# Performance work log

Hardware: AMD Instinct MI355X
Metric: run time of the kernel (lower is better)

Reference implementation:

```python
import jax, jax.numpy as jnp
import numpy as np

N_NODES = 200000
N_EDGES = 6400000
N_GRAPHS = 512
VOCAB = 10
EMBED = 8
RLEN = 20
EPS = 1e-5


def setup_inputs() -> dict:
    key = jax.random.key(0)
    ks = jax.random.split(key, 16)
    f = lambda i, shape, s: jax.random.normal(ks[i], shape, jnp.float32) * s
    return {
        "x": jax.random.normal(ks[0], (N_NODES, 3), jnp.float32),
        "W1": f(1, (3, 64), 0.5), "b1": jnp.zeros((64,), jnp.float32),
        "gamma1": jnp.ones((64,), jnp.float32), "beta1": jnp.zeros((64,), jnp.float32),
        "W2": f(2, (64, 64), 0.12), "b2": jnp.zeros((64,), jnp.float32),
        "gamma2": jnp.ones((64,), jnp.float32), "beta2": jnp.zeros((64,), jnp.float32),
        "emb": f(3, (VOCAB, EMBED), 1.0),
        "conv_w": f(4, (16, EMBED, 3), 0.2), "conv_b": jnp.zeros((16,), jnp.float32),
        "fc_w": f(5, (16 * RLEN, 64), 0.06), "fc_b": jnp.zeros((64,), jnp.float32),
        "m1_w": f(6, (192, 128), 0.08), "m1_b": jnp.zeros((128,), jnp.float32),
        "m2_w": f(7, (128, 64), 0.1), "m2_b": jnp.zeros((64,), jnp.float32),
        "m3_w": f(8, (64, 3), 0.17), "m3_b": jnp.zeros((3,), jnp.float32),
        "edge_index": jax.random.randint(ks[9], (2, N_EDGES), 0, N_NODES),
        "batch": jnp.sort(jax.random.randint(ks[10], (N_NODES,), 0, N_GRAPHS)),
        "recipe": jax.random.randint(ks[11], (N_GRAPHS, RLEN), 0, VOCAB),
    }


def _gcn_aggregate(h, src, dst, dinv, n):
    # symmetric-normalized scatter-add: sum_j (d_i d_j)^{-1/2} h_j
    norm = dinv[src] * dinv[dst]
    return jax.ops.segment_sum(h[src] * norm[:, None], dst, num_segments=n)


def _bn(h, gamma, beta):
    mu = h.mean(0)
    var = h.var(0)  # biased variance, as torch BN uses for normalization
    return (h - mu) * jax.lax.rsqrt(var + EPS) * gamma + beta


def reference(x, W1, b1, gamma1, beta1, W2, b2, gamma2, beta2, emb,
              conv_w, conv_b, fc_w, fc_b, m1_w, m1_b, m2_w, m2_b, m3_w, m3_b,
              edge_index, batch, recipe):
    n = x.shape[0]
    loop = jnp.arange(n)
    src = jnp.concatenate([edge_index[0], loop])  # add self loops (GCNConv default)
    dst = jnp.concatenate([edge_index[1], loop])
    deg = jax.ops.segment_sum(jnp.ones_like(src, jnp.float32), dst, num_segments=n)
    dinv = jnp.where(deg > 0, jax.lax.rsqrt(deg), 0.0)

    h = _gcn_aggregate(x @ W1, src, dst, dinv, n) + b1
    h = jax.nn.relu(_bn(h, gamma1, beta1))
    h = _gcn_aggregate(h @ W2, src, dst, dinv, n) + b2
    h = jax.nn.relu(_bn(h, gamma2, beta2))

    counts = jax.ops.segment_sum(jnp.ones((n,), jnp.float32), batch, num_segments=N_GRAPHS)
    h_mean = jax.ops.segment_sum(h, batch, num_segments=N_GRAPHS) / jnp.maximum(counts, 1.0)[:, None]
    h_max = jax.ops.segment_max(h, batch, num_segments=N_GRAPHS)
    h_max = jnp.where(jnp.isfinite(h_max), h_max, 0.0)  # guard empty graphs
    h_graph = jnp.concatenate([h_mean, h_max], axis=1)  # [G, 128]

    r = emb[recipe].transpose(0, 2, 1)  # [G, embed, L]
    rc = jax.lax.conv_general_dilated(r, conv_w, window_strides=(1,), padding=[(1, 1)],
                                      dimension_numbers=("NCH", "OIH", "NCH"))
    rc = jax.nn.relu(rc + conv_b[None, :, None])  # [G, 16, L]
    r_flat = rc.reshape(rc.shape[0], -1)  # channel-major flatten, matches torch
    r_vec = jax.nn.relu(r_flat @ fc_w + fc_b)  # [G, 64]

    c = jnp.concatenate([h_graph, r_vec], axis=1)  # [G, 192]
    c = jax.nn.relu(c @ m1_w + m1_b)
    c = jax.nn.relu(c @ m2_w + m2_b)
    return c @ m3_w + m3_b  # [G, 3]
```

## Files before the change

### kernel.cpp

```cpp
#include <hip/hip_runtime.h>

#define N_NODES 200000
#define N_EDGES 6400000
#define N_GRAPHS 512
#define RLEN 20
#define EMBED 8
#define EPS 1e-5f

#define NPB 1024
#define NBKT ((N_NODES + NPB - 1) / NPB)
#define CHUNK 4096

typedef unsigned short ushort_t;
typedef __attribute__((ext_vector_type(8))) short short8;
typedef __attribute__((ext_vector_type(4))) float f32x4;

__device__ inline ushort_t f32_to_bf16(float f) {
  unsigned u = __float_as_uint(f);
  unsigned r = (u + 0x7fff + ((u >> 16) & 1)) >> 16;
  return (ushort_t)r;
}
__device__ inline float bf16_to_f32(ushort_t us) {
  return __uint_as_float(((unsigned)us) << 16);
}
__device__ inline float bfu_lo(unsigned u) { return __uint_as_float(u << 16); }
__device__ inline float bfu_hi(unsigned u) { return __uint_as_float(u & 0xFFFF0000u); }


__global__ void k_bcount(const int* __restrict__ dst, int* __restrict__ bcnt) {
  __shared__ int hist[NBKT];
  for (int i = threadIdx.x; i < NBKT; i += blockDim.x) hist[i] = 0;
  __syncthreads();
  for (int e = blockIdx.x * blockDim.x + threadIdx.x; e < N_EDGES; e += gridDim.x * blockDim.x)
    atomicAdd(&hist[dst[e] >> 10], 1);
  __syncthreads();
  for (int i = threadIdx.x; i < NBKT; i += blockDim.x)
    if (hist[i]) atomicAdd(&bcnt[i], hist[i]);
}

__global__ void k_bscan(const int* __restrict__ bcnt, int* __restrict__ bstart,
                        int* __restrict__ bcursor, int* __restrict__ rowstart) {
  __shared__ int sb[256];
  int t = threadIdx.x;
  int v = (t < NBKT) ? bcnt[t] : 0;
  sb[t] = v;
  __syncthreads();
  for (int off = 1; off < 256; off <<= 1) {
    int u = (t >= off) ? sb[t - off] : 0;
    __syncthreads();
    sb[t] += u;
    __syncthreads();
  }
  if (t < NBKT) {
    int excl = sb[t] - v;
    bstart[t] = excl;
    bcursor[t] = excl;
  }
  if (t == 0) { bstart[NBKT] = N_EDGES; rowstart[N_NODES] = N_EDGES; }
}

__global__ void __launch_bounds__(256) k_bscatter(const int* __restrict__ src,
                                                  const int* __restrict__ dst,
                                                  int* __restrict__ bcursor,
                                                  int* __restrict__ ebuf) {
  __shared__ int hist[256];
  __shared__ int scanb[256];
  __shared__ int gbase[NBKT];
  __shared__ int staged[CHUNK];
  __shared__ int addrs[CHUNK];
  __shared__ int s_total;
  int t = threadIdx.x;
  int e0 = blockIdx.x * CHUNK;
  hist[t] = 0;
  __syncthreads();

  int pk[16], bk[16], rk[16];
  #pragma unroll
  for (int k = 0; k < 16; ++k) {
    int idx = e0 + t + k * 256;
    bk[k] = -1;
    if (idx < N_EDGES) {
      int s = src[idx], d = dst[idx];
      int b = d >> 10;
      pk[k] = s | ((d & (NPB - 1)) << 18);
      bk[k] = b;
      rk[k] = atomicAdd(&hist[b], 1);
    }
  }
  __syncthreads();
  int hv = hist[t];
  scanb[t] = hv;
  __syncthreads();
  for (int off = 1; off < 256; off <<= 1) {
    int u = (t >= off) ? scanb[t - off] : 0;
    __syncthreads();
    scanb[t] += u;
    __syncthreads();
  }
  int offt = scanb[t] - hv;
  if (t < NBKT && hv > 0) gbase[t] = atomicAdd(&bcursor[t], hv);
  if (t == 255) s_total = scanb[255];
  __syncthreads();
  hist[t] = offt;
  __syncthreads();
  #pragma unroll
  for (int k = 0; k < 16; ++k) {
    if (bk[k] >= 0) {
      int slot = hist[bk[k]] + rk[k];
      staged[slot] = pk[k];
      addrs[slot] = gbase[bk[k]] + rk[k];
    }
  }
  __syncthreads();
  int total = s_total;
  for (int i = t; i < total; i += 256)
    ebuf[addrs[i]] = staged[i];
}

__global__ void __launch_bounds__(256) k_bfill(const int* __restrict__ bstart,
                                               const int* __restrict__ ebuf,
                                               const float* __restrict__ x,
                                               int* __restrict__ rowstart,
                                               float* __restrict__ dinv,
                                               float4* __restrict__ xs,
                                               int* __restrict__ cols) {
  __shared__ int deg[NPB];
  __shared__ int cur[NPB];
  __shared__ int wsum[4];
  int b = blockIdx.x;
  int t = threadIdx.x;
  int lane = t & 63, wid = t >> 6;
  int estart = bstart[b], eend = bstart[b + 1];
  for (int i = t; i < NPB; i += 256) deg[i] = 0;
  __syncthreads();
  for (int i = estart + t; i < eend; i += 256) {
    int p = ebuf[i];
    atomicAdd(&deg[((unsigned)p) >> 18], 1);
  }
  __syncthreads();
  int d0 = deg[t * 4], d1 = deg[t * 4 + 1], d2 = deg[t * 4 + 2], d3 = deg[t * 4 + 3];
  int tsum = d0 + d1 + d2 + d3;
  int incl = tsum;
  #pragma unroll
  for (int off = 1; off < 64; off <<= 1) {
    int u = __shfl_up(incl, off);
    if (lane >= off) incl += u;
  }
  if (lane == 63) wsum[wid] = incl;
  int wexcl = incl - tsum;
  __syncthreads();
  int wbase = 0;
  for (int w = 0; w < wid; ++w) wbase += wsum[w];
  int ebase = wbase + wexcl;
  cur[t * 4 + 0] = ebase;
  cur[t * 4 + 1] = ebase + d0;
  cur[t * 4 + 2] = ebase + d0 + d1;
  cur[t * 4 + 3] = ebase + d0 + d1 + d2;
  __syncthreads();
  #pragma unroll
  for (int k = 0; k < 4; ++k) {
    int dl = t * 4 + k;
    int n = b * NPB + dl;
    if (n < N_NODES) {
      rowstart[n] = estart + cur[dl];
      float dv = rsqrtf((float)(deg[dl] + 1));
      dinv[n] = dv;
      float4 v;
      v.x = x[n * 3 + 0] * dv;
      v.y = x[n * 3 + 1] * dv;
      v.z = x[n * 3 + 2] * dv;
      v.w = 0.f;
      xs[n] = v;
    }
  }
  __syncthreads();
  for (int i = estart + t; i < eend; i += 256) {
    int p = ebuf[i];
    int dl = ((unsigned)p) >> 18;
    int lpos = atomicAdd(&cur[dl], 1);
    cols[estart + lpos] = p & 0x3FFFF;
  }
}


__global__ void k_agg1(const float4* __restrict__ xs, float4* __restrict__ t,
                       const int* __restrict__ rowstart, const int* __restrict__ cols,
                       const float* __restrict__ dinv) {
  int n = blockIdx.x * blockDim.x + threadIdx.x;
  if (n >= N_NODES) return;
  float4 self = xs[n];
  float a0 = self.x, a1 = self.y, a2 = self.z;
  float b0 = 0.f, b1 = 0.f, b2 = 0.f;
  float c0 = 0.f, c1 = 0.f, c2 = 0.f;
  float e0 = 0.f, e1 = 0.f, e2 = 0.f;
  int base = rowstart[n];
  int len = rowstart[n + 1] - base;
  int j = 0;
  for (; j + 4 <= len; j += 4) {
    int s0 = cols[base + j], s1 = cols[base + j + 1];
    int s2 = cols[base + j + 2], s3 = cols[base + j + 3];
    float4 v0 = xs[s0], v1 = xs[s1], v2 = xs[s2], v3 = xs[s3];
    a0 += v0.x; a1 += v0.y; a2 += v0.z;
    b0 += v1.x; b1 += v1.y; b2 += v1.z;
    c0 += v2.x; c1 += v2.y; c2 += v2.z;
    e0 += v3.x; e1 += v3.y; e2 += v3.z;
  }
  for (; j < len; ++j) {
    float4 v = xs[cols[base + j]];
    a0 += v.x; a1 += v.y; a2 += v.z;
  }
  float dv = dinv[n];
  float4 o;
  o.x = dv * ((a0 + b0) + (c0 + e0));
  o.y = dv * ((a1 + b1) + (c1 + e1));
  o.z = dv * ((a2 + b2) + (c2 + e2));
  o.w = 0.f;
  t[n] = o;
}

__global__ void k_mom(const float4* __restrict__ t, float* __restrict__ mom) {
  float m[9] = {0.f, 0.f, 0.f, 0.f, 0.f, 0.f, 0.f, 0.f, 0.f};
  for (int n = blockIdx.x * blockDim.x + threadIdx.x; n < N_NODES; n += gridDim.x * blockDim.x) {
    float4 v = t[n];
    m[0] += v.x; m[1] += v.y; m[2] += v.z;
    m[3] += v.x * v.x; m[4] += v.x * v.y; m[5] += v.x * v.z;
    m[6] += v.y * v.y; m[7] += v.y * v.z; m[8] += v.z * v.z;
  }
  #pragma unroll
  for (int off = 32; off; off >>= 1) {
    #pragma unroll
    for (int i = 0; i < 9; ++i) m[i] += __shfl_xor(m[i], off);
  }
  __shared__ float ls[4][9];
  int lane = threadIdx.x & 63, wid = threadIdx.x >> 6;
  if (lane == 0) {
    #pragma unroll
    for (int i = 0; i < 9; ++i) ls[wid][i] = m[i];
  }
  __syncthreads();
  if (threadIdx.x < 9) {
    float s = ls[0][threadIdx.x] + ls[1][threadIdx.x] + ls[2][threadIdx.x] + ls[3][threadIdx.x];
    atomicAdd(&mom[threadIdx.x], s);
  }
}

__global__ void __launch_bounds__(256) k_l2m2(const float4* __restrict__ t,
                                              ushort_t* __restrict__ hb,
                                              const float* __restrict__ W1,
                                              const float* __restrict__ W2,
                                              const float* __restrict__ mom,
                                              const float* __restrict__ gamma,
                                              const float* __restrict__ beta,
                                              const float* __restrict__ dinv) {
  __shared__ float w1s[192];
  __shared__ ushort_t w2t_hi[64 * 64];
  __shared__ ushort_t w2t_lo[64 * 64];
  __shared__ float tt[4][16][4];
  __shared__ ushort_t at_hi[4][16 * 64];
  __shared__ ushort_t at_lo[4][16 * 64];
  int tix = threadIdx.x;
  int lane = tix & 63, wid = tix >> 6;
  if (tix < 192) w1s[tix] = W1[tix];
  for (int i = tix; i < 64 * 64; i += 256) {
    int f = i >> 6, k = i & 63;
    float w = W2[k * 64 + f];
    ushort_t hi = f32_to_bf16(w);
    w2t_hi[i] = hi;
    w2t_lo[i] = f32_to_bf16(w - bf16_to_f32(hi));
  }
  __syncthreads();

  int col = lane & 15, kb = lane >> 4;
  short8 bhi[4][2], blo[4][2];
  #pragma unroll
  for (int nt = 0; nt < 4; ++nt) {
    #pragma unroll
    for (int ks = 0; ks < 2; ++ks) {
      int base = (nt * 16 + col) * 64 + ks * 32 + kb * 8;
      bhi[nt][ks] = *reinterpret_cast<const short8*>(&w2t_hi[base]);
      blo[nt][ks] = *reinterpret_cast<const short8*>(&w2t_lo[base]);
    }
  }

  float inv_n = 1.0f / N_NODES;
  float w0 = w1s[lane], w1 = w1s[64 + lane], w2 = w1s[128 + lane];
  float mu = (mom[0] * w0 + mom[1] * w1 + mom[2] * w2) * inv_n;
  float eh2 = (mom[3] * w0 * w0 + 2.f * mom[4] * w0 * w1 + 2.f * mom[5] * w0 * w2 +
               mom[6] * w1 * w1 + 2.f * mom[7] * w1 * w2 + mom[8] * w2 * w2) * inv_n;
  float var = eh2 - mu * mu;
  float sc = rsqrtf(var + EPS) * gamma[lane];
  float sh = beta[lane] - mu * sc;

  for (int bt = blockIdx.x; bt < 3125; bt += gridDim.x) {
    int n0 = (bt * 4 + wid) * 16;
    if (lane < 16) {
      float4 v = t[n0 + lane];
      tt[wid][lane][0] = v.x; tt[wid][lane][1] = v.y; tt[wid][lane][2] = v.z;
    }
    #pragma unroll 4
    for (int i = 0; i < 16; ++i) {
      float h = tt[wid][i][0] * w0 + tt[wid][i][1] * w1 + tt[wid][i][2] * w2;
      float a = h * sc + sh;
      a = a > 0.f ? a : 0.f;
      ushort_t hi = f32_to_bf16(a);
      at_hi[wid][i * 64 + lane] = hi;
      at_lo[wid][i * 64 + lane] = f32_to_bf16(a - bf16_to_f32(hi));
    }
    short8 ahi[2], alo[2];
    #pragma unroll
    for (int ks = 0; ks < 2; ++ks) {
      int base = col * 64 + ks * 32 + kb * 8;
      ahi[ks] = *reinterpret_cast<const short8*>(&at_hi[wid][base]);
      alo[ks] = *reinterpret_cast<const short8*>(&at_lo[wid][base]);
    }
    float dv[4];
    #pragma unroll
    for (int r = 0; r < 4; ++r) dv[r] = dinv[n0 + kb * 4 + r];

    #pragma unroll
    for (int nt = 0; nt < 4; ++nt) {
      f32x4 acc = {0.f, 0.f, 0.f, 0.f};
      #pragma unroll
      for (int ks = 0; ks < 2; ++ks) {
        acc = __builtin_amdgcn_mfma_f32_16x16x32_bf16(ahi[ks], bhi[nt][ks], acc, 0, 0, 0);
        acc = __builtin_amdgcn_mfma_f32_16x16x32_bf16(ahi[ks], blo[nt][ks], acc, 0, 0, 0);
        acc = __builtin_amdgcn_mfma_f32_16x16x32_bf16(alo[ks], bhi[nt][ks], acc, 0, 0, 0);
      }
      #pragma unroll
      for (int r = 0; r < 4; ++r) {
        int node = n0 + kb * 4 + r;
        int feat = nt * 16 + col;
        hb[node * 64 + feat] = f32_to_bf16(acc[r] * dv[r]);
      }
    }
  }
}

__global__ void k_agg2(const ushort_t* __restrict__ hb, float* __restrict__ hout,
                       const int* __restrict__ rowstart, const int* __restrict__ cols,
                       const float* __restrict__ dinv) {
  int node = blockIdx.x * 4 + (threadIdx.x >> 6);
  int lane = threadIdx.x & 63;
  if (node >= N_NODES) return;
  int half = lane >> 5;
  int fl = lane & 31;
  const unsigned* hb32 = (const unsigned*)hb;
  float2 acc;
  if (half == 0) {
    unsigned u = hb32[node * 32 + fl];
    acc.x = bfu_lo(u); acc.y = bfu_hi(u);
  } else { acc.x = 0.f; acc.y = 0.f; }
  int base = rowstart[node];
  int len = rowstart[node + 1] - base;
  for (int c0 = 0; c0 < len; c0 += 64) {
    int rem = len - c0;
    int m = rem < 64 ? rem : 64;
    int cidx = (lane < m) ? cols[base + c0 + lane] : 0;
    int j = 0;
    for (; j + 8 <= m; j += 8) {
      int sA = __shfl(cidx, j + half);
      int sB = __shfl(cidx, j + 2 + half);
      int sC = __shfl(cidx, j + 4 + half);
      int sD = __shfl(cidx, j + 6 + half);
      unsigned uA = hb32[sA * 32 + fl], uB = hb32[sB * 32 + fl];
      unsigned uC = hb32[sC * 32 + fl], uD = hb32[sD * 32 + fl];
      acc.x += (bfu_lo(uA) + bfu_lo(uB)) + (bfu_lo(uC) + bfu_lo(uD));
      acc.y += (bfu_hi(uA) + bfu_hi(uB)) + (bfu_hi(uC) + bfu_hi(uD));
    }
    for (; j + 2 <= m; j += 2) {
      int s = __shfl(cidx, j + half);
      unsigned u = hb32[s * 32 + fl];
      acc.x += bfu_lo(u);
      acc.y += bfu_hi(u);
    }
    if (j < m) {
      int s = __shfl(cidx, j);
      if (half == 0) {
        unsigned u = hb32[s * 32 + fl];
        acc.x += bfu_lo(u);
        acc.y += bfu_hi(u);
      }
    }
  }
  acc.x += __shfl_xor(acc.x, 32);
  acc.y += __shfl_xor(acc.y, 32);
  if (half == 0) {
    float dv = dinv[node];
    float2 o; o.x = acc.x * dv; o.y = acc.y * dv;
    ((float2*)hout)[node * 32 + fl] = o;
  }
}

__global__ void k_bnstats(const float* __restrict__ h, float* __restrict__ stats) {
  __shared__ float ls[4][64], ls2[4][64];
  int lane = threadIdx.x & 63, wid = threadIdx.x >> 6;
  float s = 0.f, s2 = 0.f;
  for (int r = blockIdx.x * 4 + wid; r < N_NODES; r += gridDim.x * 4) {
    float v = h[r * 64 + lane];
    s += v;
    s2 += v * v;
  }
  ls[wid][lane] = s;
  ls2[wid][lane] = s2;
  __syncthreads();
  if (wid == 0) {
    float a = ls[0][lane] + ls[1][lane] + ls[2][lane] + ls[3][lane];
    float b = ls2[0][lane] + ls2[1][lane] + ls2[2][lane] + ls2[3][lane];
    atomicAdd(&stats[lane], a);
    atomicAdd(&stats[64 + lane], b);
  }
}


__global__ void k_gstart(const int* __restrict__ batch, int* __restrict__ gstart) {
  int g = blockIdx.x * blockDim.x + threadIdx.x;
  if (g > N_GRAPHS) return;
  int lo = 0, hi = N_NODES;
  while (lo < hi) {
    int mid = (lo + hi) >> 1;
    if (batch[mid] < g) lo = mid + 1; else hi = mid;
  }
  gstart[g] = lo;
}

__global__ void k_pool(const float* __restrict__ h2, const float* __restrict__ stats2,
                       const float* __restrict__ gamma, const float* __restrict__ beta,
                       const int* __restrict__ gstart, float* __restrict__ hgraph) {
  __shared__ float ssum[4][64], smax[4][64];
  int g = blockIdx.x;
  int lane = threadIdx.x & 63, wid = threadIdx.x >> 6;
  int s0 = gstart[g], s1 = gstart[g + 1];
  float mu = stats2[lane] * (1.0f / N_NODES);
  float var = stats2[64 + lane] * (1.0f / N_NODES) - mu * mu;
  float sc = rsqrtf(var + EPS) * gamma[lane];
  float sh = beta[lane] - mu * sc;
  float sum = 0.f, mx = 0.f;
  for (int r = s0 + wid; r < s1; r += 4) {
    float v = h2[r * 64 + lane] * sc + sh;
    v = v > 0.f ? v : 0.f;
    sum += v;
    mx = v > mx ? v : mx;
  }
  ssum[wid][lane] = sum;
  smax[wid][lane] = mx;
  __syncthreads();
  if (wid == 0) {
    float s = ssum[0][lane] + ssum[1][lane] + ssum[2][lane] + ssum[3][lane];
    float m = fmaxf(fmaxf(smax[0][lane], smax[1][lane]), fmaxf(smax[2][lane], smax[3][lane]));
    int cnt = s1 - s0;
    float inv = 1.0f / (float)(cnt > 0 ? cnt : 1);
    hgraph[g * 128 + lane] = s * inv;
    hgraph[g * 128 + 64 + lane] = m;
  }
}

__global__ void k_head(const float* __restrict__ hgraph,
                       const float* __restrict__ emb, const int* __restrict__ recipe,
                       const float* __restrict__ conv_w, const float* __restrict__ conv_b,
                       const float* __restrict__ fc_w, const float* __restrict__ fc_b,
                       const float* __restrict__ m1_w, const float* __restrict__ m1_b,
                       const float* __restrict__ m2_w, const float* __restrict__ m2_b,
                       const float* __restrict__ m3_w, const float* __restrict__ m3_b,
                       float* __restrict__ out) {
  __shared__ float r_s[RLEN][EMBED];
  __shared__ float convout[16 * RLEN];
  __shared__ float cvec[192];
  __shared__ float y1[128];
  __shared__ float y2[64];
  __shared__ int rec_s[RLEN];
  __shared__ float emb_s[80];
  int g = blockIdx.x;
  int t = threadIdx.x;
  if (t < 80) emb_s[t] = emb[t];
  if (t < RLEN) rec_s[t] = recipe[g * RLEN + t];
  __syncthreads();
  for (int idx = t; idx < RLEN * EMBED; idx += blockDim.x) {
    int pos = idx >> 3, e = idx & 7;
    r_s[pos][e] = emb_s[rec_s[pos] * EMBED + e];
  }
  if (t < 128) cvec[t] = hgraph[g * 128 + t];
  __syncthreads();
  for (int idx = t; idx < 16 * RLEN; idx += blockDim.x) {
    int c = idx / RLEN, pos = idx % RLEN;
    float acc = conv_b[c];
    #pragma unroll
    for (int k = 0; k < 3; ++k) {
      int p = pos + k - 1;
      if (p >= 0 && p < RLEN) {
        #pragma unroll
        for (int e = 0; e < EMBED; ++e)
          acc = fmaf(r_s[p][e], conv_w[(c * EMBED + e) * 3 + k], acc);
      }
    }
    convout[c * RLEN + pos] = acc > 0.f ? acc : 0.f;
  }
  __syncthreads();
  if (t < 64) {
    float acc = fc_b[t];
    for (int i = 0; i < 320; ++i) acc = fmaf(convout[i], fc_w[i * 64 + t], acc);
    cvec[128 + t] = acc > 0.f ? acc : 0.f;
  }
  __syncthreads();
  if (t < 128) {
    float acc = m1_b[t];
    for (int i = 0; i < 192; ++i) acc = fmaf(cvec[i], m1_w[i * 128 + t], acc);
    y1[t] = acc > 0.f ? acc : 0.f;
  }
  __syncthreads();
  if (t < 64) {
    float acc = m2_b[t];
    for (int i = 0; i < 128; ++i) acc = fmaf(y1[i], m2_w[i * 64 + t], acc);
    y2[t] = acc > 0.f ? acc : 0.f;
  }
  __syncthreads();
  if (t < 3) {
    float acc = m3_b[t];
    for (int i = 0; i < 64; ++i) acc = fmaf(y2[i], m3_w[i * 3 + t], acc);
    out[g * 3 + t] = acc;
  }
}

extern "C" void kernel_launch(void* const* d_in, const int* in_sizes, int n_in,
                              void* d_out, int out_size, void* d_ws, size_t ws_size,
                              hipStream_t stream) {
  const float* x      = (const float*)d_in[0];
  const float* W1     = (const float*)d_in[1];
  const float* gamma1 = (const float*)d_in[3];
  const float* beta1  = (const float*)d_in[4];
  const float* W2     = (const float*)d_in[5];
  const float* gamma2 = (const float*)d_in[7];
  const float* beta2  = (const float*)d_in[8];
  const float* emb    = (const float*)d_in[9];
  const float* conv_w = (const float*)d_in[10];
  const float* conv_b = (const float*)d_in[11];
  const float* fc_w   = (const float*)d_in[12];
  const float* fc_b   = (const float*)d_in[13];
  const float* m1_w   = (const float*)d_in[14];
  const float* m1_b   = (const float*)d_in[15];
  const float* m2_w   = (const float*)d_in[16];
  const float* m2_b   = (const float*)d_in[17];
  const float* m3_w   = (const float*)d_in[18];
  const float* m3_b   = (const float*)d_in[19];
  const int* ei       = (const int*)d_in[20];
  const int* batch    = (const int*)d_in[21];
  const int* recipe   = (const int*)d_in[22];
  const int* e_src = ei;
  const int* e_dst = ei + N_EDGES;
  float* out = (float*)d_out;

  char* p = (char*)d_ws;
  auto alloc = [&](size_t bytes) {
    char* r = p;
    p += (bytes + 255) & ~(size_t)255;
    return (void*)r;
  };
  int*   bcnt     = (int*)alloc((size_t)NBKT * 4);
  int*   bstart   = (int*)alloc((size_t)(NBKT + 1) * 4);
  int*   bcursor  = (int*)alloc((size_t)NBKT * 4);
  float* dinv     = (float*)alloc((size_t)N_NODES * 4);
  int*   rowstart = (int*)alloc((size_t)(N_NODES + 1) * 4);
  int*   gstart   = (int*)alloc((size_t)(N_GRAPHS + 1) * 4);
  float* stats    = (float*)alloc(256 * 4);
  float* mom      = (float*)alloc(16 * 4);
  float* hgraph   = (float*)alloc((size_t)N_GRAPHS * 128 * 4);
  int*   cols     = (int*)alloc((size_t)N_EDGES * 4);
  float4* xs      = (float4*)alloc((size_t)N_NODES * 16);
  float4* tbuf    = (float4*)alloc((size_t)N_NODES * 16);
  float* h1       = (float*)alloc((size_t)N_NODES * 64 * 4);
  ushort_t* hb    = (ushort_t*)alloc((size_t)N_NODES * 64 * 2);
  int*   ebuf     = (int*)h1;

  hipMemsetAsync(bcnt, 0, (size_t)NBKT * 4, stream);
  hipMemsetAsync(stats, 0, 256 * 4, stream);
  hipMemsetAsync(mom, 0, 16 * 4, stream);

  k_bcount<<<512, 256, 0, stream>>>(e_dst, bcnt);
  k_bscan<<<1, 256, 0, stream>>>(bcnt, bstart, bcursor, rowstart);
  k_bscatter<<<(N_EDGES + CHUNK - 1) / CHUNK, 256, 0, stream>>>(e_src, e_dst, bcursor, ebuf);
  k_bfill<<<NBKT, 256, 0, stream>>>(bstart, ebuf, x, rowstart, dinv, xs, cols);
  k_agg1<<<(N_NODES + 255) / 256, 256, 0, stream>>>(xs, tbuf, rowstart, cols, dinv);
  k_mom<<<256, 256, 0, stream>>>(tbuf, mom);
  k_l2m2<<<625, 256, 0, stream>>>(tbuf, hb, W1, W2, mom, gamma1, beta1, dinv);
  k_agg2<<<(N_NODES + 3) / 4, 256, 0, stream>>>(hb, h1, rowstart, cols, dinv);
  k_bnstats<<<512, 256, 0, stream>>>(h1, stats);
  k_gstart<<<1, 576, 0, stream>>>(batch, gstart);
  k_pool<<<N_GRAPHS, 256, 0, stream>>>(h1, stats, gamma2, beta2, gstart, hgraph);
  k_head<<<N_GRAPHS, 128, 0, stream>>>(hgraph, emb, recipe, conv_w, conv_b, fc_w, fc_b,
                                       m1_w, m1_b, m2_w, m2_b, m3_w, m3_b, out);
}
```

Baseline: 485.9 us.

## Fuse BN statistics into aggregation kernels and store layer-2 output as bf16

Folds the first-layer moment reduction into k_agg1 and the second-layer BN sum/sumsq reduction into k_agg2, which becomes a grid-stride kernel with 2048 blocks. The layer-2 output is stored as bf16 instead of fp32, halving its write and the reads in pooling. The gather loops are unrolled further to keep more loads in flight. This drops two kernel launches and a full pass over the 51 MB activation, at the cost of bf16 rounding of the pre-BN activations and per-block atomics.

```diff
diff --git a/kernel.cpp b/kernel.cpp
--- a/kernel.cpp
+++ b/kernel.cpp
@@ -185,57 +185,64 @@
 
 __global__ void k_agg1(const float4* __restrict__ xs, float4* __restrict__ t,
                        const int* __restrict__ rowstart, const int* __restrict__ cols,
-                       const float* __restrict__ dinv) {
+                       const float* __restrict__ dinv, float* __restrict__ mom) {
   int n = blockIdx.x * blockDim.x + threadIdx.x;
-  if (n >= N_NODES) return;
-  float4 self = xs[n];
-  float a0 = self.x, a1 = self.y, a2 = self.z;
-  float b0 = 0.f, b1 = 0.f, b2 = 0.f;
-  float c0 = 0.f, c1 = 0.f, c2 = 0.f;
-  float e0 = 0.f, e1 = 0.f, e2 = 0.f;
-  int base = rowstart[n];
-  int len = rowstart[n + 1] - base;
-  int j = 0;
-  for (; j + 4 <= len; j += 4) {
-    int s0 = cols[base + j], s1 = cols[base + j + 1];
-    int s2 = cols[base + j + 2], s3 = cols[base + j + 3];
-    float4 v0 = xs[s0], v1 = xs[s1], v2 = xs[s2], v3 = xs[s3];
-    a0 += v0.x; a1 += v0.y; a2 += v0.z;
-    b0 += v1.x; b1 += v1.y; b2 += v1.z;
-    c0 += v2.x; c1 += v2.y; c2 += v2.z;
-    e0 += v3.x; e1 += v3.y; e2 += v3.z;
-  }
-  for (; j < len; ++j) {
-    float4 v = xs[cols[base + j]];
-    a0 += v.x; a1 += v.y; a2 += v.z;
-  }
-  float dv = dinv[n];
-  float4 o;
-  o.x = dv * ((a0 + b0) + (c0 + e0));
-  o.y = dv * ((a1 + b1) + (c1 + e1));
-  o.z = dv * ((a2 + b2) + (c2 + e2));
-  o.w = 0.f;
-  t[n] = o;
-}
-
-__global__ void k_mom(const float4* __restrict__ t, float* __restrict__ mom) {
-  float m[9] = {0.f, 0.f, 0.f, 0.f, 0.f, 0.f, 0.f, 0.f, 0.f};
-  for (int n = blockIdx.x * blockDim.x + threadIdx.x; n < N_NODES; n += gridDim.x * blockDim.x) {
-    float4 v = t[n];
-    m[0] += v.x; m[1] += v.y; m[2] += v.z;
-    m[3] += v.x * v.x; m[4] += v.x * v.y; m[5] += v.x * v.z;
-    m[6] += v.y * v.y; m[7] += v.y * v.z; m[8] += v.z * v.z;
+  float m9[9] = {0.f, 0.f, 0.f, 0.f, 0.f, 0.f, 0.f, 0.f, 0.f};
+  if (n < N_NODES) {
+    float4 self = xs[n];
+    float a0 = self.x, a1 = self.y, a2 = self.z;
+    float b0 = 0.f, b1 = 0.f, b2 = 0.f;
+    float c0 = 0.f, c1 = 0.f, c2 = 0.f;
+    float e0 = 0.f, e1 = 0.f, e2 = 0.f;
+    int base = rowstart[n];
+    int len = rowstart[n + 1] - base;
+    int j = 0;
+    for (; j + 8 <= len; j += 8) {
+      int s0 = cols[base + j],     s1 = cols[base + j + 1];
+      int s2 = cols[base + j + 2], s3 = cols[base + j + 3];
+      int s4 = cols[base + j + 4], s5 = cols[base + j + 5];
+      int s6 = cols[base + j + 6], s7 = cols[base + j + 7];
+      float4 v0 = xs[s0], v1 = xs[s1], v2 = xs[s2], v3 = xs[s3];
+      float4 v4 = xs[s4], v5 = xs[s5], v6 = xs[s6], v7 = xs[s7];
+      a0 += v0.x + v4.x; a1 += v0.y + v4.y; a2 += v0.z + v4.z;
+      b0 += v1.x + v5.x; b1 += v1.y + v5.y; b2 += v1.z + v5.z;
+      c0 += v2.x + v6.x; c1 += v2.y + v6.y; c2 += v2.z + v6.z;
+      e0 += v3.x + v7.x; e1 += v3.y + v7.y; e2 += v3.z + v7.z;
+    }
+    for (; j + 4 <= len; j += 4) {
+      int s0 = cols[base + j], s1 = cols[base + j + 1];
+      int s2 = cols[base + j + 2], s3 = cols[base + j + 3];
+      float4 v0 = xs[s0], v1 = xs[s1], v2 = xs[s2], v3 = xs[s3];
+      a0 += v0.x; a1 += v0.y; a2 += v0.z;
+      b0 += v1.x; b1 += v1.y; b2 += v1.z;
+      c0 += v2.x; c1 += v2.y; c2 += v2.z;
+      e0 += v3.x; e1 += v3.y; e2 += v3.z;
+    }
+    for (; j < len; ++j) {
+      float4 v = xs[cols[base + j]];
+      a0 += v.x; a1 += v.y; a2 += v.z;
+    }
+    float dv = dinv[n];
+    float4 o;
+    o.x = dv * ((a0 + b0) + (c0 + e0));
+    o.y = dv * ((a1 + b1) + (c1 + e1));
+    o.z = dv * ((a2 + b2) + (c2 + e2));
+    o.w = 0.f;
+    t[n] = o;
+    m9[0] = o.x; m9[1] = o.y; m9[2] = o.z;
+    m9[3] = o.x * o.x; m9[4] = o.x * o.y; m9[5] = o.x * o.z;
+    m9[6] = o.y * o.y; m9[7] = o.y * o.z; m9[8] = o.z * o.z;
   }
   #pragma unroll
   for (int off = 32; off; off >>= 1) {
     #pragma unroll
-    for (int i = 0; i < 9; ++i) m[i] += __shfl_xor(m[i], off);
+    for (int i = 0; i < 9; ++i) m9[i] += __shfl_xor(m9[i], off);
   }
   __shared__ float ls[4][9];
   int lane = threadIdx.x & 63, wid = threadIdx.x >> 6;
   if (lane == 0) {
     #pragma unroll
-    for (int i = 0; i < 9; ++i) ls[wid][i] = m[i];
+    for (int i = 0; i < 9; ++i) ls[wid][i] = m9[i];
   }
   __syncthreads();
   if (threadIdx.x < 9) {
@@ -336,78 +343,87 @@
   }
 }
 
-__global__ void k_agg2(const ushort_t* __restrict__ hb, float* __restrict__ hout,
+__global__ void __launch_bounds__(256) k_agg2(const ushort_t* __restrict__ hb,
+                       ushort_t* __restrict__ h1b,
                        const int* __restrict__ rowstart, const int* __restrict__ cols,
-                       const float* __restrict__ dinv) {
-  int node = blockIdx.x * 4 + (threadIdx.x >> 6);
-  int lane = threadIdx.x & 63;
-  if (node >= N_NODES) return;
-  int half = lane >> 5;
-  int fl = lane & 31;
+                       const float* __restrict__ dinv, float* __restrict__ stats) {
+  int tid = threadIdx.x;
+  int lane = tid & 63, wid = tid >> 6;
+  int half = lane >> 5, fl = lane & 31;
   const unsigned* hb32 = (const unsigned*)hb;
-  float2 acc;
-  if (half == 0) {
-    unsigned u = hb32[node * 32 + fl];
-    acc.x = bfu_lo(u); acc.y = bfu_hi(u);
-  } else { acc.x = 0.f; acc.y = 0.f; }
-  int base = rowstart[node];
-  int len = rowstart[node + 1] - base;
-  for (int c0 = 0; c0 < len; c0 += 64) {
-    int rem = len - c0;
-    int m = rem < 64 ? rem : 64;
-    int cidx = (lane < m) ? cols[base + c0 + lane] : 0;
-    int j = 0;
-    for (; j + 8 <= m; j += 8) {
-      int sA = __shfl(cidx, j + half);
-      int sB = __shfl(cidx, j + 2 + half);
-      int sC = __shfl(cidx, j + 4 + half);
-      int sD = __shfl(cidx, j + 6 + half);
-      unsigned uA = hb32[sA * 32 + fl], uB = hb32[sB * 32 + fl];
-      unsigned uC = hb32[sC * 32 + fl], uD = hb32[sD * 32 + fl];
-      acc.x += (bfu_lo(uA) + bfu_lo(uB)) + (bfu_lo(uC) + bfu_lo(uD));
-      acc.y += (bfu_hi(uA) + bfu_hi(uB)) + (bfu_hi(uC) + bfu_hi(uD));
-    }
-    for (; j + 2 <= m; j += 2) {
-      int s = __shfl(cidx, j + half);
-      unsigned u = hb32[s * 32 + fl];
-      acc.x += bfu_lo(u);
-      acc.y += bfu_hi(u);
-    }
-    if (j < m) {
-      int s = __shfl(cidx, j);
-      if (half == 0) {
+  unsigned* h1b32 = (unsigned*)h1b;
+  float s0 = 0.f, s1 = 0.f, q0 = 0.f, q1 = 0.f;
+  for (int node = blockIdx.x * 4 + wid; node < N_NODES; node += gridDim.x * 4) {
+    float2 acc;
+    if (half == 0) {
+      unsigned u = hb32[node * 32 + fl];
+      acc.x = bfu_lo(u); acc.y = bfu_hi(u);
+    } else { acc.x = 0.f; acc.y = 0.f; }
+    int base = rowstart[node];
+    int len = rowstart[node + 1] - base;
+    for (int c0 = 0; c0 < len; c0 += 64) {
+      int rem = len - c0;
+      int m = rem < 64 ? rem : 64;
+      int cidx = (lane < m) ? cols[base + c0 + lane] : 0;
+      int j = 0;
+      for (; j + 16 <= m; j += 16) {
+        int sA = __shfl(cidx, j + half),      sB = __shfl(cidx, j + 2 + half);
+        int sC = __shfl(cidx, j + 4 + half),  sD = __shfl(cidx, j + 6 + half);
+        int sE = __shfl(cidx, j + 8 + half),  sF = __shfl(cidx, j + 10 + half);
+        int sG = __shfl(cidx, j + 12 + half), sH = __shfl(cidx, j + 14 + half);
+        unsigned uA = hb32[sA * 32 + fl], uB = hb32[sB * 32 + fl];
+        unsigned uC = hb32[sC * 32 + fl], uD = hb32[sD * 32 + fl];
+        unsigned uE = hb32[sE * 32 + fl], uF = hb32[sF * 32 + fl];
+        unsigned uG = hb32[sG * 32 + fl], uH = hb32[sH * 32 + fl];
+        acc.x += ((bfu_lo(uA) + bfu_lo(uB)) + (bfu_lo(uC) + bfu_lo(uD)))
+               + ((bfu_lo(uE) + bfu_lo(uF)) + (bfu_lo(uG) + bfu_lo(uH)));
+        acc.y += ((bfu_hi(uA) + bfu_hi(uB)) + (bfu_hi(uC) + bfu_hi(uD)))
+               + ((bfu_hi(uE) + bfu_hi(uF)) + (bfu_hi(uG) + bfu_hi(uH)));
+      }
+      for (; j + 8 <= m; j += 8) {
+        int sA = __shfl(cidx, j + half),     sB = __shfl(cidx, j + 2 + half);
+        int sC = __shfl(cidx, j + 4 + half), sD = __shfl(cidx, j + 6 + half);
+        unsigned uA = hb32[sA * 32 + fl], uB = hb32[sB * 32 + fl];
+        unsigned uC = hb32[sC * 32 + fl], uD = hb32[sD * 32 + fl];
+        acc.x += (bfu_lo(uA) + bfu_lo(uB)) + (bfu_lo(uC) + bfu_lo(uD));
+        acc.y += (bfu_hi(uA) + bfu_hi(uB)) + (bfu_hi(uC) + bfu_hi(uD));
+      }
+      for (; j + 2 <= m; j += 2) {
+        int s = __shfl(cidx, j + half);
         unsigned u = hb32[s * 32 + fl];
         acc.x += bfu_lo(u);
         acc.y += bfu_hi(u);
       }
-    }
-  }
-  acc.x += __shfl_xor(acc.x, 32);
-  acc.y += __shfl_xor(acc.y, 32);
+      if (j < m) {
+        int s = __shfl(cidx, j);
+        if (half == 0) {
+          unsigned u = hb32[s * 32 + fl];
+          acc.x += bfu_lo(u);
+          acc.y += bfu_hi(u);
+        }
+      }
+    }
+    acc.x += __shfl_xor(acc.x, 32);
+    acc.y += __shfl_xor(acc.y, 32);
+    if (half == 0) {
+      float dv = dinv[node];
+      float ox = acc.x * dv, oy = acc.y * dv;
+      h1b32[node * 32 + fl] = ((unsigned)f32_to_bf16(oy) << 16) | (unsigned)f32_to_bf16(ox);
+      s0 += ox; s1 += oy;
+      q0 += ox * ox; q1 += oy * oy;
+    }
+  }
+  __shared__ float lsum[4][64], lsq[4][64];
   if (half == 0) {
-    float dv = dinv[node];
-    float2 o; o.x = acc.x * dv; o.y = acc.y * dv;
-    ((float2*)hout)[node * 32 + fl] = o;
-  }
-}
-
-__global__ void k_bnstats(const float* __restrict__ h, float* __restrict__ stats) {
-  __shared__ float ls[4][64], ls2[4][64];
-  int lane = threadIdx.x & 63, wid = threadIdx.x >> 6;
-  float s = 0.f, s2 = 0.f;
-  for (int r = blockIdx.x * 4 + wid; r < N_NODES; r += gridDim.x * 4) {
-    float v = h[r * 64 + lane];
-    s += v;
-    s2 += v * v;
-  }
-  ls[wid][lane] = s;
-  ls2[wid][lane] = s2;
-  __syncthreads();
-  if (wid == 0) {
-    float a = ls[0][lane] + ls[1][lane] + ls[2][lane] + ls[3][lane];
-    float b = ls2[0][lane] + ls2[1][lane] + ls2[2][lane] + ls2[3][lane];
-    atomicAdd(&stats[lane], a);
-    atomicAdd(&stats[64 + lane], b);
+    lsum[wid][2 * fl] = s0; lsum[wid][2 * fl + 1] = s1;
+    lsq[wid][2 * fl] = q0;  lsq[wid][2 * fl + 1] = q1;
+  }
+  __syncthreads();
+  if (tid < 64) {
+    float a = lsum[0][tid] + lsum[1][tid] + lsum[2][tid] + lsum[3][tid];
+    float b = lsq[0][tid] + lsq[1][tid] + lsq[2][tid] + lsq[3][tid];
+    atomicAdd(&stats[tid], a);
+    atomicAdd(&stats[64 + tid], b);
   }
 }
 
@@ -423,7 +439,7 @@
   gstart[g] = lo;
 }
 
-__global__ void k_pool(const float* __restrict__ h2, const float* __restrict__ stats2,
+__global__ void k_pool(const ushort_t* __restrict__ h1b, const float* __restrict__ stats2,
                        const float* __restrict__ gamma, const float* __restrict__ beta,
                        const int* __restrict__ gstart, float* __restrict__ hgraph) {
   __shared__ float ssum[4][64], smax[4][64];
@@ -436,7 +452,7 @@
   float sh = beta[lane] - mu * sc;
   float sum = 0.f, mx = 0.f;
   for (int r = s0 + wid; r < s1; r += 4) {
-    float v = h2[r * 64 + lane] * sc + sh;
+    float v = bf16_to_f32(h1b[r * 64 + lane]) * sc + sh;
     v = v > 0.f ? v : 0.f;
     sum += v;
     mx = v > mx ? v : mx;
@@ -566,9 +582,9 @@
   int*   cols     = (int*)alloc((size_t)N_EDGES * 4);
   float4* xs      = (float4*)alloc((size_t)N_NODES * 16);
   float4* tbuf    = (float4*)alloc((size_t)N_NODES * 16);
-  float* h1       = (float*)alloc((size_t)N_NODES * 64 * 4);
+  ushort_t* h1b   = (ushort_t*)alloc((size_t)N_NODES * 64 * 2);
   ushort_t* hb    = (ushort_t*)alloc((size_t)N_NODES * 64 * 2);
-  int*   ebuf     = (int*)h1;
+  int*   ebuf     = (int*)h1b;
 
   hipMemsetAsync(bcnt, 0, (size_t)NBKT * 4, stream);
   hipMemsetAsync(stats, 0, 256 * 4, stream);
@@ -578,13 +594,11 @@
   k_bscan<<<1, 256, 0, stream>>>(bcnt, bstart, bcursor, rowstart);
   k_bscatter<<<(N_EDGES + CHUNK - 1) / CHUNK, 256, 0, stream>>>(e_src, e_dst, bcursor, ebuf);
   k_bfill<<<NBKT, 256, 0, stream>>>(bstart, ebuf, x, rowstart, dinv, xs, cols);
-  k_agg1<<<(N_NODES + 255) / 256, 256, 0, stream>>>(xs, tbuf, rowstart, cols, dinv);
-  k_mom<<<256, 256, 0, stream>>>(tbuf, mom);
+  k_agg1<<<(N_NODES + 255) / 256, 256, 0, stream>>>(xs, tbuf, rowstart, cols, dinv, mom);
   k_l2m2<<<625, 256, 0, stream>>>(tbuf, hb, W1, W2, mom, gamma1, beta1, dinv);
-  k_agg2<<<(N_NODES + 3) / 4, 256, 0, stream>>>(hb, h1, rowstart, cols, dinv);
-  k_bnstats<<<512, 256, 0, stream>>>(h1, stats);
+  k_agg2<<<2048, 256, 0, stream>>>(hb, h1b, rowstart, cols, dinv, stats);
   k_gstart<<<1, 576, 0, stream>>>(batch, gstart);
-  k_pool<<<N_GRAPHS, 256, 0, stream>>>(h1, stats, gamma2, beta2, gstart, hgraph);
+  k_pool<<<N_GRAPHS, 256, 0, stream>>>(h1b, stats, gamma2, beta2, gstart, hgraph);
   k_head<<<N_GRAPHS, 128, 0, stream>>>(hgraph, emb, recipe, conv_w, conv_b, fc_w, fc_b,
                                        m1_w, m1_b, m2_w, m2_b, m3_w, m3_b, out);
 }
```

New measurement: 464.2 us. -4.5%, faster.
